# Kernel tuning notes

Hardware: AMD Instinct MI355X
Metric: run time of the kernel (lower is better)

The kernel has to match this reference:

```python
import jax, jax.numpy as jnp
import numpy as np

B, S, D_MODEL, H = 2, 2048, 1024, 16
HD = D_MODEL // H  # 64


def rotate_half(x):
    # pairs (x_even, x_odd) -> (-x_odd, x_even), interleaved back
    x1 = x[..., ::2]
    x2 = x[..., 1::2]
    return jnp.stack([-x2, x1], axis=-1).reshape(x.shape)


def rope_sin_cos(seq_len, head_dim):
    pos = jnp.arange(seq_len, dtype=jnp.float32)
    dim = jnp.arange(head_dim, dtype=jnp.float32)
    theta = 10000.0 ** (-2.0 * jnp.floor(dim / 2.0) / head_dim)
    angles = pos[:, None] * theta[None, :]  # [S, HD]
    return jnp.sin(angles), jnp.cos(angles)


def setup_inputs():
    key = jax.random.key(0)
    ks = jax.random.split(key, 6)
    w_scale = 1.0 / np.sqrt(D_MODEL)
    x = jax.random.normal(ks[0], (B, S, D_MODEL), jnp.float32)
    # causal mask: 1.0 where attention is disallowed (j > i)
    mask = (1.0 - jnp.tril(jnp.ones((S, S), jnp.float32)))[None, None, :, :]
    wq = jax.random.normal(ks[1], (D_MODEL, D_MODEL), jnp.float32) * w_scale
    wk = jax.random.normal(ks[2], (D_MODEL, D_MODEL), jnp.float32) * w_scale
    wv = jax.random.normal(ks[3], (D_MODEL, D_MODEL), jnp.float32) * w_scale
    wo = jax.random.normal(ks[4], (D_MODEL, D_MODEL), jnp.float32) * w_scale
    zeros = jnp.zeros((D_MODEL,), jnp.float32)
    return dict(x=x, mask=mask, wq=wq, bq=zeros, wk=wk, bk=zeros,
                wv=wv, bv=zeros, wo=wo, bo=zeros)


def reference(x, mask, wq, bq, wk, bk, wv, bv, wo, bo):
    b, s, _ = x.shape

    def split_heads(t):  # [B,S,D] -> [B,H,S,HD]
        return t.reshape(b, s, H, HD).transpose(0, 2, 1, 3)

    q = split_heads(x @ wq + bq)
    k = split_heads(x @ wk + bk)
    v = split_heads(x @ wv + bv)

    sin, cos = rope_sin_cos(s, HD)
    sin = sin[None, None, :, :]
    cos = cos[None, None, :, :]
    q = q * cos + rotate_half(q) * sin
    k = k * cos + rotate_half(k) * sin

    logits = jnp.einsum('bhqd,bhkd->bhqk', q, k) / jnp.sqrt(jnp.float32(HD))
    logits = logits + mask * (-1e9)
    attn = jax.nn.softmax(logits, axis=-1)
    out = jnp.einsum('bhqk,bhkd->bhqd', attn, v)  # [B,H,S,HD]
    out = out.transpose(0, 2, 1, 3).reshape(b, s, D_MODEL)
    return out @ wo + bo
```

## Files before the change

### kernel.cpp

```cpp
#include <hip/hip_runtime.h>
#include <hip/hip_bf16.h>


#define S_ 2048
#define DM 1024
#define HD 64

typedef __attribute__((ext_vector_type(8))) short short8;
typedef __attribute__((ext_vector_type(4))) float floatx4;

__device__ __forceinline__ unsigned short f2b(float x) {
  union { __hip_bfloat16 h; unsigned short u; } cv;
  cv.h = __float2bfloat16(x);
  return cv.u;
}

__device__ __forceinline__ void gload_lds16(const unsigned short* g, unsigned short* l) {
  typedef const __attribute__((address_space(1))) unsigned int* gp_t;
  typedef __attribute__((address_space(3))) unsigned int* lp_t;
  __builtin_amdgcn_global_load_lds((gp_t)(const void*)g, (lp_t)(void*)l, 16, 0, 0);
}

__global__ void cast_kernel(const float* __restrict__ in,
                            unsigned short* __restrict__ out, int n) {
  int i = (blockIdx.x * blockDim.x + threadIdx.x) * 4;
  if (i >= n) return;
  float4 v = *(const float4*)(in + i);
  ushort4 o;
  o.x = f2b(v.x); o.y = f2b(v.y); o.z = f2b(v.z); o.w = f2b(v.w);
  *(ushort4*)(out + i) = o;
}

__global__ void trans_kernel(const float* __restrict__ w0, const float* __restrict__ w1,
                             const float* __restrict__ w2, const float* __restrict__ w3,
                             unsigned short* __restrict__ wt) {
  __shared__ float tile[32][33];
  const float* W = (blockIdx.z == 0) ? w0 : (blockIdx.z == 1) ? w1
                   : (blockIdx.z == 2) ? w2 : w3;
  unsigned short* Wt = wt + (size_t)blockIdx.z * DM * DM;
  const int tx = threadIdx.x & 31;
  const int ty = threadIdx.x >> 5;
  const int k0 = blockIdx.x * 32;
  const int c0 = blockIdx.y * 32;
#pragma unroll
  for (int i = 0; i < 4; ++i)
    tile[ty + i * 8][tx] = W[(size_t)(k0 + ty + i * 8) * DM + c0 + tx];
  __syncthreads();
#pragma unroll
  for (int i = 0; i < 4; ++i)
    Wt[(size_t)(c0 + ty + i * 8) * DM + k0 + tx] = f2b(tile[tx][ty + i * 8]);
}

__global__ void rope_kernel(float2* __restrict__ tab) {
  int i = blockIdx.x * 256 + threadIdx.x;
  int s = i >> 5, d2 = i & 31;
  float th = expf(-(float)d2 * (9.210340371976184f / 32.0f));
  float sn, cs;
  sincosf((float)s * th, &sn, &cs);
  tab[i] = make_float2(cs, sn);
}

__global__ __launch_bounds__(256, 3) void gemm_qkv(
    const unsigned short* __restrict__ A, const unsigned short* __restrict__ Wt,
    const float* __restrict__ bq, const float* __restrict__ bk,
    const float* __restrict__ bv, const float2* __restrict__ rope,
    unsigned short* __restrict__ QKV) {
  __shared__ __attribute__((aligned(16))) unsigned short As[128 * 32];
  __shared__ __attribute__((aligned(16))) unsigned short Bs[128 * 32];
  const int r0 = blockIdx.x * 128;
  const int c0 = blockIdx.y * 128;
  const int t = threadIdx.x;
  const int lane = t & 63;
  const int wv = t >> 6;
  const int wr = (wv >> 1) * 64;
  const int wc = (wv & 1) * 64;
  const int lr = lane & 15;
  const int lg = lane >> 4;

  const int srow = wv * 32 + (lane >> 2);
  const int sseg = (lane & 3) * 8;
  const unsigned short* Ag = A + (size_t)(r0 + srow) * DM + sseg;
  const unsigned short* Bg = Wt + (size_t)(c0 + srow) * DM + sseg;
  unsigned short* lA = &As[wv * 1024];
  unsigned short* lB = &Bs[wv * 1024];

  floatx4 acc[4][4] = {};

  for (int k0 = 0; k0 < DM; k0 += 32) {
    gload_lds16(Ag + k0, lA);
    gload_lds16(Ag + k0 + 16 * DM, lA + 512);
    gload_lds16(Bg + k0, lB);
    gload_lds16(Bg + k0 + 16 * DM, lB + 512);
    __syncthreads();
    short8 af[4], bf[4];
#pragma unroll
    for (int m = 0; m < 4; ++m)
      af[m] = *(const short8*)(&As[(wr + m * 16 + lr) * 32 + lg * 8]);
#pragma unroll
    for (int n = 0; n < 4; ++n)
      bf[n] = *(const short8*)(&Bs[(wc + n * 16 + lr) * 32 + lg * 8]);
#pragma unroll
    for (int m = 0; m < 4; ++m)
#pragma unroll
      for (int n = 0; n < 4; ++n)
        acc[m][n] = __builtin_amdgcn_mfma_f32_16x16x32_bf16(af[m], bf[n], acc[m][n], 0, 0, 0);
    __syncthreads();
  }

  const int mat = blockIdx.y >> 3;
  const float* bias = (mat == 0) ? bq : (mat == 1) ? bk : bv;
  const int rbase = r0 + wr + lg * 4;
  const int cbase = c0 + wc + lr;
#pragma unroll
  for (int n = 0; n < 4; ++n) {
    const int c = cbase + n * 16;
    const int cc = c & (DM - 1);
    const float bvv = bias[cc];
    const int d = c & 63;
    const int h = cc >> 6;
#pragma unroll
    for (int m = 0; m < 4; ++m) {
#pragma unroll
      for (int i = 0; i < 4; ++i) {
        const int r = rbase + m * 16 + i;
        const int s = r & (S_ - 1);
        const int b = r >> 11;
        float v = acc[m][n][i] + bvv;
        float pv = __shfl_xor(v, 1);
        if (mat < 2) {
          float2 cssn = rope[s * 32 + (d >> 1)];
          v = (d & 1) ? fmaf(v, cssn.x, pv * cssn.y) : fmaf(v, cssn.x, -pv * cssn.y);
          if (mat == 0) v *= 0.18033688011112042f;
        }
        QKV[((size_t)((mat << 5) | (b << 4) | h) * S_ + s) * HD + d] = f2b(v);
      }
    }
  }
}

__global__ __launch_bounds__(256, 3) void gemm_out(
    const unsigned short* __restrict__ A, const unsigned short* __restrict__ Wt,
    const float* __restrict__ bias, float* __restrict__ out) {
  __shared__ __attribute__((aligned(16))) unsigned short As[128 * 32];
  __shared__ __attribute__((aligned(16))) unsigned short Bs[128 * 32];
  const int r0 = blockIdx.x * 128;
  const int c0 = blockIdx.y * 128;
  const int t = threadIdx.x;
  const int lane = t & 63;
  const int wv = t >> 6;
  const int wr = (wv >> 1) * 64;
  const int wc = (wv & 1) * 64;
  const int lr = lane & 15;
  const int lg = lane >> 4;

  const int srow = wv * 32 + (lane >> 2);
  const int sseg = (lane & 3) * 8;
  const unsigned short* Ag = A + (size_t)(r0 + srow) * DM + sseg;
  const unsigned short* Bg = Wt + (size_t)(c0 + srow) * DM + sseg;
  unsigned short* lA = &As[wv * 1024];
  unsigned short* lB = &Bs[wv * 1024];

  floatx4 acc[4][4] = {};

  for (int k0 = 0; k0 < DM; k0 += 32) {
    gload_lds16(Ag + k0, lA);
    gload_lds16(Ag + k0 + 16 * DM, lA + 512);
    gload_lds16(Bg + k0, lB);
    gload_lds16(Bg + k0 + 16 * DM, lB + 512);
    __syncthreads();
    short8 af[4], bf[4];
#pragma unroll
    for (int m = 0; m < 4; ++m)
      af[m] = *(const short8*)(&As[(wr + m * 16 + lr) * 32 + lg * 8]);
#pragma unroll
    for (int n = 0; n < 4; ++n)
      bf[n] = *(const short8*)(&Bs[(wc + n * 16 + lr) * 32 + lg * 8]);
#pragma unroll
    for (int m = 0; m < 4; ++m)
#pragma unroll
      for (int n = 0; n < 4; ++n)
        acc[m][n] = __builtin_amdgcn_mfma_f32_16x16x32_bf16(af[m], bf[n], acc[m][n], 0, 0, 0);
    __syncthreads();
  }

  const int rbase = r0 + wr + lg * 4;
  const int cbase = c0 + wc + lr;
#pragma unroll
  for (int n = 0; n < 4; ++n) {
    const int c = cbase + n * 16;
    const float bvv = bias[c];
#pragma unroll
    for (int m = 0; m < 4; ++m) {
#pragma unroll
      for (int i = 0; i < 4; ++i) {
        const int r = rbase + m * 16 + i;
        out[(size_t)r * DM + c] = acc[m][n][i] + bvv;
      }
    }
  }
}

__global__ __launch_bounds__(256, 4) void attn_kernel(
    const unsigned short* __restrict__ Q, const unsigned short* __restrict__ K,
    const unsigned short* __restrict__ V, unsigned short* __restrict__ AttnC) {
  __shared__ __attribute__((aligned(16))) unsigned short Ks[2][64 * 64];
  __shared__ __attribute__((aligned(16))) unsigned short Vs[2][64 * 64];
  __shared__ __attribute__((aligned(16))) unsigned short Ps[4][16 * 64];

  const int bh = blockIdx.x;
  const int qt = (int)(gridDim.y - 1) - (int)blockIdx.y;
  const int tid = threadIdx.x;
  const int w = tid >> 6;
  const int l = tid & 63;
  const int lg = l >> 4;
  const int lr = l & 15;
  const size_t base = (size_t)bh * S_ * HD;

  short8 qf[2];
  {
    const unsigned short* Qrow = Q + base + (size_t)(qt * 64 + w * 16 + lr) * HD + lg * 8;
    qf[0] = *(const short8*)(Qrow);
    qf[1] = *(const short8*)(Qrow + 32);
  }

  floatx4 o[4] = {};
  float m = -1e30f, lsum = 0.f;

  const int krow = tid >> 3;
  const int kseg = tid & 7;
  const int oct = tid >> 5;
  const int kp = tid & 31;

  int4 kr0, kr1; short8 va, vb;
  {
    const unsigned short* Kg = K + base;
    const unsigned short* Vg = V + base;
    kr0 = *(const int4*)(Kg + krow * 64 + kseg * 8);
    kr1 = *(const int4*)(Kg + (krow + 32) * 64 + kseg * 8);
    va = *(const short8*)(Vg + (2 * kp) * 64 + oct * 8);
    vb = *(const short8*)(Vg + (2 * kp + 1) * 64 + oct * 8);
  }

  char* const Pw = (char*)Ps[w];
  const int pswz = (lr & 7) << 4;

  for (int t = 0; t <= qt; ++t) {
    const int cur = t & 1;
    {
      char* Kb = (char*)Ks[cur];
      *(int4*)(Kb + krow * 128 + ((kseg * 16) ^ ((krow & 7) << 4))) = kr0;
      *(int4*)(Kb + (krow + 32) * 128 + ((kseg * 16) ^ ((krow & 7) << 4))) = kr1;
      char* Vb = (char*)Vs[cur];
#pragma unroll
      for (int j = 0; j < 8; ++j) {
        int d = oct * 8 + j;
        unsigned int pk = (unsigned int)(unsigned short)va[j] |
                          ((unsigned int)(unsigned short)vb[j] << 16);
        *(unsigned int*)(Vb + d * 128 + ((4 * kp) ^ (j << 4))) = pk;
      }
    }
    if (t < qt) {
      const unsigned short* Kg = K + base + (size_t)(t + 1) * 64 * HD;
      const unsigned short* Vg = V + base + (size_t)(t + 1) * 64 * HD;
      kr0 = *(const int4*)(Kg + krow * 64 + kseg * 8);
      kr1 = *(const int4*)(Kg + (krow + 32) * 64 + kseg * 8);
      va = *(const short8*)(Vg + (2 * kp) * 64 + oct * 8);
      vb = *(const short8*)(Vg + (2 * kp + 1) * 64 + oct * 8);
    }
    __syncthreads();

    floatx4 s[4] = {};
    __builtin_amdgcn_s_setprio(1);
#pragma unroll
    for (int kk = 0; kk < 2; ++kk) {
#pragma unroll
      for (int n = 0; n < 4; ++n) {
        int r = n * 16 + lr;
        short8 kf = *(const short8*)((char*)Ks[cur] + r * 128 +
                                     ((kk * 64 + lg * 16) ^ ((r & 7) << 4)));
        s[n] = __builtin_amdgcn_mfma_f32_16x16x32_bf16(kf, qf[kk], s[n], 0, 0, 0);
      }
    }
    __builtin_amdgcn_s_setprio(0);
    if (t == qt) {
#pragma unroll
      for (int n = 0; n < 4; ++n)
#pragma unroll
        for (int i = 0; i < 4; ++i)
          if (n * 16 + lg * 4 + i > w * 16 + lr) s[n][i] = -1e30f;
    }

    float tm0 = fmaxf(fmaxf(s[0][0], s[0][1]), fmaxf(s[0][2], s[0][3]));
    float tm1 = fmaxf(fmaxf(s[1][0], s[1][1]), fmaxf(s[1][2], s[1][3]));
    float tm2 = fmaxf(fmaxf(s[2][0], s[2][1]), fmaxf(s[2][2], s[2][3]));
    float tm3 = fmaxf(fmaxf(s[3][0], s[3][1]), fmaxf(s[3][2], s[3][3]));
    float tm = fmaxf(fmaxf(tm0, tm1), fmaxf(tm2, tm3));
    tm = fmaxf(tm, __shfl_xor(tm, 16));
    tm = fmaxf(tm, __shfl_xor(tm, 32));
    const float mn = fmaxf(m, tm);
    const float al = exp2f(m - mn);
    m = mn;
    float ps = 0.f;
#pragma unroll
    for (int n = 0; n < 4; ++n) {
#pragma unroll
      for (int i = 0; i < 4; ++i) {
        float p = exp2f(s[n][i] - mn);
        s[n][i] = p;
        ps += p;
      }
    }
    lsum = lsum * al + ps;
#pragma unroll
    for (int dd = 0; dd < 4; ++dd) o[dd] *= al;

#pragma unroll
    for (int n = 0; n < 4; ++n) {
#pragma unroll
      for (int h = 0; h < 2; ++h) {
        unsigned int pk = (unsigned int)f2b(s[n][2 * h]) |
                          ((unsigned int)f2b(s[n][2 * h + 1]) << 16);
        *(unsigned int*)(Pw + lr * 128 + (((n * 16 + lg * 4 + 2 * h) * 2) ^ pswz)) = pk;
      }
    }
    short8 pb[2];
#pragma unroll
    for (int kk = 0; kk < 2; ++kk)
      pb[kk] = *(const short8*)(Pw + lr * 128 + ((kk * 64 + lg * 16) ^ pswz));
    __builtin_amdgcn_s_setprio(1);
#pragma unroll
    for (int kk = 0; kk < 2; ++kk)
#pragma unroll
      for (int dd = 0; dd < 4; ++dd) {
        int d = dd * 16 + lr;
        short8 vbf = *(const short8*)((char*)Vs[cur] + d * 128 +
                                      ((kk * 64 + lg * 16) ^ ((d & 7) << 4)));
        o[dd] = __builtin_amdgcn_mfma_f32_16x16x32_bf16(vbf, pb[kk], o[dd], 0, 0, 0);
      }
    __builtin_amdgcn_s_setprio(0);
  }

  lsum += __shfl_xor(lsum, 16);
  lsum += __shfl_xor(lsum, 32);
  const float inv = 1.f / lsum;
  unsigned short* orow =
      AttnC + (size_t)((bh >> 4) * S_ + qt * 64 + w * 16 + lr) * DM + (bh & 15) * HD;
#pragma unroll
  for (int dd = 0; dd < 4; ++dd) {
    unsigned int w0 = (unsigned int)f2b(o[dd][0] * inv) |
                      ((unsigned int)f2b(o[dd][1] * inv) << 16);
    unsigned int w1 = (unsigned int)f2b(o[dd][2] * inv) |
                      ((unsigned int)f2b(o[dd][3] * inv) << 16);
    *(uint2*)(orow + dd * 16 + lg * 4) = make_uint2(w0, w1);
  }
}

extern "C" void kernel_launch(void* const* d_in, const int* in_sizes, int n_in,
                              void* d_out, int out_size, void* d_ws, size_t ws_size,
                              hipStream_t stream) {
  const float* x = (const float*)d_in[0];
  const float* wq = (const float*)d_in[2];
  const float* bq = (const float*)d_in[3];
  const float* wk = (const float*)d_in[4];
  const float* bk = (const float*)d_in[5];
  const float* wv = (const float*)d_in[6];
  const float* bv = (const float*)d_in[7];
  const float* wo = (const float*)d_in[8];
  const float* bo = (const float*)d_in[9];

  char* ws = (char*)d_ws;
  const size_t MB = 1024ull * 1024ull;
  unsigned short* Xc = (unsigned short*)(ws);
  unsigned short* Wt = (unsigned short*)(ws + 8 * MB);
  unsigned short* QKVb = (unsigned short*)(ws + 16 * MB);
  unsigned short* Ac = (unsigned short*)(ws + 40 * MB);
  float2* rope = (float2*)(ws + 48 * MB);

  cast_kernel<<<4096, 256, 0, stream>>>(x, Xc, 2 * S_ * DM);
  trans_kernel<<<dim3(32, 32, 4), 256, 0, stream>>>(wq, wk, wv, wo, Wt);
  rope_kernel<<<256, 256, 0, stream>>>(rope);
  gemm_qkv<<<dim3(32, 24), 256, 0, stream>>>(Xc, Wt, bq, bk, bv, rope, QKVb);
  attn_kernel<<<dim3(32, 32), 256, 0, stream>>>(
      QKVb, QKVb + 32ull * S_ * HD, QKVb + 64ull * S_ * HD, Ac);
  gemm_out<<<dim3(32, 8), 256, 0, stream>>>(Ac, Wt + 3ull * DM * DM, bo, (float*)d_out);
}
```

Measured before the change: 127.6 us.

## Widen GEMM K-tile with swizzled LDS, enlarge attention blocks, lazy softmax rescale

After: 120.5 us. 1.06x faster.

```diff
diff --git a/kernel.cpp b/kernel.cpp
--- a/kernel.cpp
+++ b/kernel.cpp
@@ -7,6 +7,7 @@
 #define HD 64
 
 typedef __attribute__((ext_vector_type(8))) short short8;
+typedef __attribute__((ext_vector_type(4))) short short4v;
 typedef __attribute__((ext_vector_type(4))) float floatx4;
 
 __device__ __forceinline__ unsigned short f2b(float x) {
@@ -65,8 +66,8 @@
     const float* __restrict__ bq, const float* __restrict__ bk,
     const float* __restrict__ bv, const float2* __restrict__ rope,
     unsigned short* __restrict__ QKV) {
-  __shared__ __attribute__((aligned(16))) unsigned short As[128 * 32];
-  __shared__ __attribute__((aligned(16))) unsigned short Bs[128 * 32];
+  __shared__ __attribute__((aligned(16))) unsigned short As[128 * 64];
+  __shared__ __attribute__((aligned(16))) unsigned short Bs[128 * 64];
   const int r0 = blockIdx.x * 128;
   const int c0 = blockIdx.y * 128;
   const int t = threadIdx.x;
@@ -77,33 +78,40 @@
   const int lr = lane & 15;
   const int lg = lane >> 4;
 
-  const int srow = wv * 32 + (lane >> 2);
-  const int sseg = (lane & 3) * 8;
+  const int srow = wv * 32 + (lane >> 3);
+  const int sseg = ((lane & 7) ^ (lane >> 3)) * 8;
   const unsigned short* Ag = A + (size_t)(r0 + srow) * DM + sseg;
   const unsigned short* Bg = Wt + (size_t)(c0 + srow) * DM + sseg;
-  unsigned short* lA = &As[wv * 1024];
-  unsigned short* lB = &Bs[wv * 1024];
+  unsigned short* lA = &As[wv * 32 * 64];
+  unsigned short* lB = &Bs[wv * 32 * 64];
 
   floatx4 acc[4][4] = {};
-
-  for (int k0 = 0; k0 < DM; k0 += 32) {
-    gload_lds16(Ag + k0, lA);
-    gload_lds16(Ag + k0 + 16 * DM, lA + 512);
-    gload_lds16(Bg + k0, lB);
-    gload_lds16(Bg + k0 + 16 * DM, lB + 512);
+  const int fswz = (lr & 7) << 4;
+
+  for (int k0 = 0; k0 < DM; k0 += 64) {
+#pragma unroll
+    for (int j = 0; j < 4; ++j) {
+      gload_lds16(Ag + k0 + j * 8 * DM, lA + j * 8 * 64);
+      gload_lds16(Bg + k0 + j * 8 * DM, lB + j * 8 * 64);
+    }
     __syncthreads();
-    short8 af[4], bf[4];
-#pragma unroll
-    for (int m = 0; m < 4; ++m)
-      af[m] = *(const short8*)(&As[(wr + m * 16 + lr) * 32 + lg * 8]);
-#pragma unroll
-    for (int n = 0; n < 4; ++n)
-      bf[n] = *(const short8*)(&Bs[(wc + n * 16 + lr) * 32 + lg * 8]);
-#pragma unroll
-    for (int m = 0; m < 4; ++m)
+#pragma unroll
+    for (int kk = 0; kk < 2; ++kk) {
+      short8 af[4], bf[4];
+#pragma unroll
+      for (int m = 0; m < 4; ++m)
+        af[m] = *(const short8*)((char*)As + (wr + m * 16 + lr) * 128 +
+                                 ((kk * 64 + lg * 16) ^ fswz));
 #pragma unroll
       for (int n = 0; n < 4; ++n)
-        acc[m][n] = __builtin_amdgcn_mfma_f32_16x16x32_bf16(af[m], bf[n], acc[m][n], 0, 0, 0);
+        bf[n] = *(const short8*)((char*)Bs + (wc + n * 16 + lr) * 128 +
+                                 ((kk * 64 + lg * 16) ^ fswz));
+#pragma unroll
+      for (int m = 0; m < 4; ++m)
+#pragma unroll
+        for (int n = 0; n < 4; ++n)
+          acc[m][n] = __builtin_amdgcn_mfma_f32_16x16x32_bf16(af[m], bf[n], acc[m][n], 0, 0, 0);
+    }
     __syncthreads();
   }
 
@@ -141,8 +149,8 @@
 __global__ __launch_bounds__(256, 3) void gemm_out(
     const unsigned short* __restrict__ A, const unsigned short* __restrict__ Wt,
     const float* __restrict__ bias, float* __restrict__ out) {
-  __shared__ __attribute__((aligned(16))) unsigned short As[128 * 32];
-  __shared__ __attribute__((aligned(16))) unsigned short Bs[128 * 32];
+  __shared__ __attribute__((aligned(16))) unsigned short As[128 * 64];
+  __shared__ __attribute__((aligned(16))) unsigned short Bs[128 * 64];
   const int r0 = blockIdx.x * 128;
   const int c0 = blockIdx.y * 128;
   const int t = threadIdx.x;
@@ -153,33 +161,40 @@
   const int lr = lane & 15;
   const int lg = lane >> 4;
 
-  const int srow = wv * 32 + (lane >> 2);
-  const int sseg = (lane & 3) * 8;
+  const int srow = wv * 32 + (lane >> 3);
+  const int sseg = ((lane & 7) ^ (lane >> 3)) * 8;
   const unsigned short* Ag = A + (size_t)(r0 + srow) * DM + sseg;
   const unsigned short* Bg = Wt + (size_t)(c0 + srow) * DM + sseg;
-  unsigned short* lA = &As[wv * 1024];
-  unsigned short* lB = &Bs[wv * 1024];
+  unsigned short* lA = &As[wv * 32 * 64];
+  unsigned short* lB = &Bs[wv * 32 * 64];
 
   floatx4 acc[4][4] = {};
-
-  for (int k0 = 0; k0 < DM; k0 += 32) {
-    gload_lds16(Ag + k0, lA);
-    gload_lds16(Ag + k0 + 16 * DM, lA + 512);
-    gload_lds16(Bg + k0, lB);
-    gload_lds16(Bg + k0 + 16 * DM, lB + 512);
+  const int fswz = (lr & 7) << 4;
+
+  for (int k0 = 0; k0 < DM; k0 += 64) {
+#pragma unroll
+    for (int j = 0; j < 4; ++j) {
+      gload_lds16(Ag + k0 + j * 8 * DM, lA + j * 8 * 64);
+      gload_lds16(Bg + k0 + j * 8 * DM, lB + j * 8 * 64);
+    }
     __syncthreads();
-    short8 af[4], bf[4];
-#pragma unroll
-    for (int m = 0; m < 4; ++m)
-      af[m] = *(const short8*)(&As[(wr + m * 16 + lr) * 32 + lg * 8]);
-#pragma unroll
-    for (int n = 0; n < 4; ++n)
-      bf[n] = *(const short8*)(&Bs[(wc + n * 16 + lr) * 32 + lg * 8]);
-#pragma unroll
-    for (int m = 0; m < 4; ++m)
+#pragma unroll
+    for (int kk = 0; kk < 2; ++kk) {
+      short8 af[4], bf[4];
+#pragma unroll
+      for (int m = 0; m < 4; ++m)
+        af[m] = *(const short8*)((char*)As + (wr + m * 16 + lr) * 128 +
+                                 ((kk * 64 + lg * 16) ^ fswz));
 #pragma unroll
       for (int n = 0; n < 4; ++n)
-        acc[m][n] = __builtin_amdgcn_mfma_f32_16x16x32_bf16(af[m], bf[n], acc[m][n], 0, 0, 0);
+        bf[n] = *(const short8*)((char*)Bs + (wc + n * 16 + lr) * 128 +
+                                 ((kk * 64 + lg * 16) ^ fswz));
+#pragma unroll
+      for (int m = 0; m < 4; ++m)
+#pragma unroll
+        for (int n = 0; n < 4; ++n)
+          acc[m][n] = __builtin_amdgcn_mfma_f32_16x16x32_bf16(af[m], bf[n], acc[m][n], 0, 0, 0);
+    }
     __syncthreads();
   }
 
@@ -200,25 +215,29 @@
   }
 }
 
-__global__ __launch_bounds__(256, 4) void attn_kernel(
+__global__ __launch_bounds__(512, 4) void attn_kernel(
     const unsigned short* __restrict__ Q, const unsigned short* __restrict__ K,
     const unsigned short* __restrict__ V, unsigned short* __restrict__ AttnC) {
   __shared__ __attribute__((aligned(16))) unsigned short Ks[2][64 * 64];
   __shared__ __attribute__((aligned(16))) unsigned short Vs[2][64 * 64];
-  __shared__ __attribute__((aligned(16))) unsigned short Ps[4][16 * 64];
+  __shared__ __attribute__((aligned(16))) unsigned short Ps[8][16 * 64];
 
   const int bh = blockIdx.x;
-  const int qt = (int)(gridDim.y - 1) - (int)blockIdx.y;
+  const int qt = 15 - (int)blockIdx.y;
   const int tid = threadIdx.x;
   const int w = tid >> 6;
   const int l = tid & 63;
   const int lg = l >> 4;
   const int lr = l & 15;
   const size_t base = (size_t)bh * S_ * HD;
+  const int NT = 2 * qt + 2;
+  const int dt = 2 * qt + (w >> 2);
+  const int qin = ((w & 3) << 4) + lr;
 
   short8 qf[2];
   {
-    const unsigned short* Qrow = Q + base + (size_t)(qt * 64 + w * 16 + lr) * HD + lg * 8;
+    const unsigned short* Qrow =
+        Q + base + (size_t)(qt * 128 + w * 16 + lr) * HD + lg * 8;
     qf[0] = *(const short8*)(Qrow);
     qf[1] = *(const short8*)(Qrow + 32);
   }
@@ -228,46 +247,45 @@
 
   const int krow = tid >> 3;
   const int kseg = tid & 7;
-  const int oct = tid >> 5;
   const int kp = tid & 31;
-
-  int4 kr0, kr1; short8 va, vb;
+  const int vd0 = ((tid >> 5) & 7) * 8 + (tid >> 8) * 4;
+
+  int4 kr;
+  short4v va, vb;
   {
     const unsigned short* Kg = K + base;
     const unsigned short* Vg = V + base;
-    kr0 = *(const int4*)(Kg + krow * 64 + kseg * 8);
-    kr1 = *(const int4*)(Kg + (krow + 32) * 64 + kseg * 8);
-    va = *(const short8*)(Vg + (2 * kp) * 64 + oct * 8);
-    vb = *(const short8*)(Vg + (2 * kp + 1) * 64 + oct * 8);
+    kr = *(const int4*)(Kg + krow * 64 + kseg * 8);
+    va = *(const short4v*)(Vg + 2 * kp * 64 + vd0);
+    vb = *(const short4v*)(Vg + (2 * kp + 1) * 64 + vd0);
   }
 
   char* const Pw = (char*)Ps[w];
   const int pswz = (lr & 7) << 4;
 
-  for (int t = 0; t <= qt; ++t) {
+  for (int t = 0; t < NT; ++t) {
     const int cur = t & 1;
     {
       char* Kb = (char*)Ks[cur];
-      *(int4*)(Kb + krow * 128 + ((kseg * 16) ^ ((krow & 7) << 4))) = kr0;
-      *(int4*)(Kb + (krow + 32) * 128 + ((kseg * 16) ^ ((krow & 7) << 4))) = kr1;
+      *(int4*)(Kb + krow * 128 + ((kseg * 16) ^ ((krow & 7) << 4))) = kr;
       char* Vb = (char*)Vs[cur];
 #pragma unroll
-      for (int j = 0; j < 8; ++j) {
-        int d = oct * 8 + j;
-        unsigned int pk = (unsigned int)(unsigned short)va[j] |
-                          ((unsigned int)(unsigned short)vb[j] << 16);
-        *(unsigned int*)(Vb + d * 128 + ((4 * kp) ^ (j << 4))) = pk;
-      }
-    }
-    if (t < qt) {
+      for (int jj = 0; jj < 4; ++jj) {
+        int d = vd0 + jj;
+        unsigned int pk = (unsigned int)(unsigned short)va[jj] |
+                          ((unsigned int)(unsigned short)vb[jj] << 16);
+        *(unsigned int*)(Vb + d * 128 + ((4 * kp) ^ ((d & 7) << 4))) = pk;
+      }
+    }
+    if (t + 1 < NT) {
       const unsigned short* Kg = K + base + (size_t)(t + 1) * 64 * HD;
       const unsigned short* Vg = V + base + (size_t)(t + 1) * 64 * HD;
-      kr0 = *(const int4*)(Kg + krow * 64 + kseg * 8);
-      kr1 = *(const int4*)(Kg + (krow + 32) * 64 + kseg * 8);
-      va = *(const short8*)(Vg + (2 * kp) * 64 + oct * 8);
-      vb = *(const short8*)(Vg + (2 * kp + 1) * 64 + oct * 8);
+      kr = *(const int4*)(Kg + krow * 64 + kseg * 8);
+      va = *(const short4v*)(Vg + 2 * kp * 64 + vd0);
+      vb = *(const short4v*)(Vg + (2 * kp + 1) * 64 + vd0);
     }
     __syncthreads();
+    if (t > dt) continue;
 
     floatx4 s[4] = {};
     __builtin_amdgcn_s_setprio(1);
@@ -282,12 +300,12 @@
       }
     }
     __builtin_amdgcn_s_setprio(0);
-    if (t == qt) {
+    if (t == dt) {
 #pragma unroll
       for (int n = 0; n < 4; ++n)
 #pragma unroll
         for (int i = 0; i < 4; ++i)
-          if (n * 16 + lg * 4 + i > w * 16 + lr) s[n][i] = -1e30f;
+          if (n * 16 + lg * 4 + i > qin) s[n][i] = -1e30f;
     }
 
     float tm0 = fmaxf(fmaxf(s[0][0], s[0][1]), fmaxf(s[0][2], s[0][3]));
@@ -297,22 +315,25 @@
     float tm = fmaxf(fmaxf(tm0, tm1), fmaxf(tm2, tm3));
     tm = fmaxf(tm, __shfl_xor(tm, 16));
     tm = fmaxf(tm, __shfl_xor(tm, 32));
-    const float mn = fmaxf(m, tm);
-    const float al = exp2f(m - mn);
-    m = mn;
+    if (__any(tm > m + 8.f)) {
+      const float mn = fmaxf(m, tm);
+      const float al = exp2f(m - mn);
+      m = mn;
+      lsum *= al;
+#pragma unroll
+      for (int dd = 0; dd < 4; ++dd) o[dd] *= al;
+    }
     float ps = 0.f;
 #pragma unroll
     for (int n = 0; n < 4; ++n) {
 #pragma unroll
       for (int i = 0; i < 4; ++i) {
-        float p = exp2f(s[n][i] - mn);
+        float p = exp2f(s[n][i] - m);
         s[n][i] = p;
         ps += p;
       }
     }
-    lsum = lsum * al + ps;
-#pragma unroll
-    for (int dd = 0; dd < 4; ++dd) o[dd] *= al;
+    lsum += ps;
 
 #pragma unroll
     for (int n = 0; n < 4; ++n) {
@@ -344,7 +365,7 @@
   lsum += __shfl_xor(lsum, 32);
   const float inv = 1.f / lsum;
   unsigned short* orow =
-      AttnC + (size_t)((bh >> 4) * S_ + qt * 64 + w * 16 + lr) * DM + (bh & 15) * HD;
+      AttnC + (size_t)((bh >> 4) * S_ + qt * 128 + w * 16 + lr) * DM + (bh & 15) * HD;
 #pragma unroll
   for (int dd = 0; dd < 4; ++dd) {
     unsigned int w0 = (unsigned int)f2b(o[dd][0] * inv) |
@@ -380,7 +401,7 @@
   trans_kernel<<<dim3(32, 32, 4), 256, 0, stream>>>(wq, wk, wv, wo, Wt);
   rope_kernel<<<256, 256, 0, stream>>>(rope);
   gemm_qkv<<<dim3(32, 24), 256, 0, stream>>>(Xc, Wt, bq, bk, bv, rope, QKVb);
-  attn_kernel<<<dim3(32, 32), 256, 0, stream>>>(
+  attn_kernel<<<dim3(32, 16), 512, 0, stream>>>(
       QKVb, QKVb + 32ull * S_ * HD, QKVb + 64ull * S_ * HD, Ac);
   gemm_out<<<dim3(32, 8), 256, 0, stream>>>(Ac, Wt + 3ull * DM * DM, bo, (float*)d_out);
 }
```
